# Kernel tuning notes

Measured on AMD Instinct MI355X. Metric: run time of the kernel, lower is better.

Reference implementation:

```python
import jax, jax.numpy as jnp
import numpy as np

MAX_DISP = 4  # 9x9 = 81 displacement window, stride 1


def setup_inputs() -> dict:
    key = jax.random.key(0)
    k1, k2 = jax.random.split(key)
    B, C, H, W = 4, 256, 128, 224
    first = jax.random.normal(k1, (B, C, H, W), dtype=jnp.float32)
    second = jax.random.normal(k2, (B, C, H, W), dtype=jnp.float32)
    return {"first": first, "second": second}


def reference(first, second):
    # FlowNet-style correlation: out[b, 9*dy+dx, y, x] =
    #   (1/C) * sum_c first[b,c,y,x] * second[b,c, y+dy-4, x+dx-4]
    # with zero padding outside the image (rbot buffers are zero-padded by 4).
    B, C, H, W = first.shape
    P = MAX_DISP
    sp = jnp.pad(second, ((0, 0), (0, 0), (P, P), (P, P)))  # [B,C,H+8,W+8]
    outs = []
    for dy in range(2 * P + 1):          # top channel = dy*9 + dx (dx fastest)
        for dx in range(2 * P + 1):
            shifted = sp[:, :, dy:dy + H, dx:dx + W]
            outs.append(jnp.sum(first * shifted, axis=1))  # [B,H,W]
    out = jnp.stack(outs, axis=1)  # [B,81,H,W]
    return out / jnp.float32(C)
```

## Files before the change

### kernel.cpp

```cpp
#include <hip/hip_runtime.h>

#define PAD   4
#define DD    9
#define ND    81
#define BB    4
#define CCH   256
#define HH_   128
#define WW_   224
#define TH    8
#define TW    32
#define NTILES 448
#define PLANE  (HH_*WW_)

__global__ __launch_bounds__(64)
void corr_kernel(const float* __restrict__ first,
                 const float* __restrict__ second,
                 const float* __restrict__ zws,
                 float* __restrict__ out)
{
    const int bx   = blockIdx.x;
    const int tile = bx % NTILES;
    const int dy   = bx / NTILES;
    const int wt   = tile % 7;
    const int ht   = (tile / 7) % 16;
    const int b    = tile / 112;
    const int w0   = wt * TW, h0 = ht * TH;

    const int lane = threadIdx.x;
    const int wq   = lane & 7;
    const int hh   = lane >> 3;

    const int h = h0 + hh;
    const int w = w0 + 4 * wq;
    const int srow  = h + dy - PAD;
    const bool valid = (srow >= 0) && (srow < HH_);
    const int srowc = valid ? srow : 0;

    const size_t plane = PLANE;
    const float* fbase = first  + (size_t)b * CCH * plane;
    const float* sbase = second + (size_t)b * CCH * plane;

    const float* fp = fbase + (size_t)h * WW_ + w;
    const float* sp = valid ? (sbase + (size_t)srowc * WW_ + w) : zws;
    const size_t sinc = valid ? plane : 0;

    const bool isL = (wq == 0), isR = (wq == 7);
    const int  ecol   = isL ? (w0 - PAD) : (w0 + TW);
    const bool evalid = valid && ((isL && w0 > 0) || (isR && (w0 + TW) < WW_));
    const float* ep = evalid ? (sbase + (size_t)srowc * WW_ + ecol) : zws;
    const size_t einc = evalid ? plane : 0;

    const int li = (lane + 63) & 63;
    const int ri = (lane + 1) & 63;

    float acc[DD][4];
    #pragma unroll
    for (int dx = 0; dx < DD; ++dx) { acc[dx][0]=0.f; acc[dx][1]=0.f; acc[dx][2]=0.f; acc[dx][3]=0.f; }

    float4 f = *(const float4*)fp;  fp += plane;
    float4 m = *(const float4*)sp;  sp += sinc;
    float4 e = *(const float4*)ep;  ep += einc;

    for (int c = 0; c < CCH; ++c) {
        float4 fn, mn, en;
        if (c + 1 < CCH) {
            fn = *(const float4*)fp;  fp += plane;
            mn = *(const float4*)sp;  sp += sinc;
            en = *(const float4*)ep;  ep += einc;
        } else { fn = f; mn = m; en = e; }

        float a0 = __shfl(m.x, li), a1 = __shfl(m.y, li),
              a2 = __shfl(m.z, li), a3 = __shfl(m.w, li);
        float c0 = __shfl(m.x, ri), c1 = __shfl(m.y, ri),
              c2 = __shfl(m.z, ri), c3 = __shfl(m.w, ri);
        if (isL) { a0 = e.x; a1 = e.y; a2 = e.z; a3 = e.w; }
        if (isR) { c0 = e.x; c1 = e.y; c2 = e.z; c3 = e.w; }

        const float s[12] = { a0, a1, a2, a3,
                              m.x, m.y, m.z, m.w,
                              c0, c1, c2, c3 };
        const float fv[4] = { f.x, f.y, f.z, f.w };

        #pragma unroll
        for (int dx = 0; dx < DD; ++dx)
            #pragma unroll
            for (int px = 0; px < 4; ++px)
                acc[dx][px] += fv[px] * s[dx + px];

        f = fn; m = mn; e = en;
    }

    const float inv = 1.0f / (float)CCH;
    #pragma unroll
    for (int dx = 0; dx < DD; ++dx) {
        const int d = dy * DD + dx;
        float4 o = make_float4(acc[dx][0]*inv, acc[dx][1]*inv,
                               acc[dx][2]*inv, acc[dx][3]*inv);
        *(float4*)&out[(((size_t)b * ND + d) * HH_ + h) * WW_ + w] = o;
    }
}

extern "C" void kernel_launch(void* const* d_in, const int* in_sizes, int n_in,
                              void* d_out, int out_size, void* d_ws, size_t ws_size,
                              hipStream_t stream) {
    const float* first  = (const float*)d_in[0];
    const float* second = (const float*)d_in[1];
    float* out = (float*)d_out;
    hipMemsetAsync(d_ws, 0, 256, stream);
    dim3 grid(NTILES * DD);
    dim3 block(64);
    corr_kernel<<<grid, block, 0, stream>>>(first, second, (const float*)d_ws, out);
}
```

Before: 459.9 us.

## Split the nine horizontal displacements across two wavefronts per block

Each block now runs two 64-lane wavefronts over the same pixel tile. Wave 0 computes displacements dx 0-3 and wave 1 computes dx 4-8, which cuts per-thread accumulators from 36 to 20 and raises the thread count. The cost is that both waves load the same first and second channels, roughly doubling global/L2 load traffic per output. Wave 0 also does a redundant fifth accumulator that it never stores.

```diff
diff --git a/kernel.cpp b/kernel.cpp
--- a/kernel.cpp
+++ b/kernel.cpp
@@ -12,7 +12,7 @@
 #define NTILES 448
 #define PLANE  (HH_*WW_)
 
-__global__ __launch_bounds__(64)
+__global__ __launch_bounds__(128)
 void corr_kernel(const float* __restrict__ first,
                  const float* __restrict__ second,
                  const float* __restrict__ zws,
@@ -26,7 +26,9 @@
     const int b    = tile / 112;
     const int w0   = wt * TW, h0 = ht * TH;
 
-    const int lane = threadIdx.x;
+    const int tid  = threadIdx.x;
+    const int wv   = tid >> 6;
+    const int lane = tid & 63;
     const int wq   = lane & 7;
     const int hh   = lane >> 3;
 
@@ -45,17 +47,23 @@
     const size_t sinc = valid ? plane : 0;
 
     const bool isL = (wq == 0), isR = (wq == 7);
-    const int  ecol   = isL ? (w0 - PAD) : (w0 + TW);
-    const bool evalid = valid && ((isL && w0 > 0) || (isR && (w0 + TW) < WW_));
+    const int  ecol   = wv ? (w0 + TW) : (w0 - PAD);
+    const bool evalid = valid && (wv ? (isR && (w0 + TW) < WW_)
+                                     : (isL && w0 > 0));
     const float* ep = evalid ? (sbase + (size_t)srowc * WW_ + ecol) : zws;
     const size_t einc = evalid ? plane : 0;
 
     const int li = (lane + 63) & 63;
     const int ri = (lane + 1) & 63;
 
-    float acc[DD][4];
+    const int sel_lo = wv ? lane : li;
+    const int sel_hi = wv ? ri   : lane;
+    const bool rep_lo = (wv == 0) && isL;
+    const bool rep_hi = (wv == 1) && isR;
+
+    float acc[5][4];
     #pragma unroll
-    for (int dx = 0; dx < DD; ++dx) { acc[dx][0]=0.f; acc[dx][1]=0.f; acc[dx][2]=0.f; acc[dx][3]=0.f; }
+    for (int j = 0; j < 5; ++j) { acc[j][0]=0.f; acc[j][1]=0.f; acc[j][2]=0.f; acc[j][3]=0.f; }
 
     float4 f = *(const float4*)fp;  fp += plane;
     float4 m = *(const float4*)sp;  sp += sinc;
@@ -69,33 +77,32 @@
             en = *(const float4*)ep;  ep += einc;
         } else { fn = f; mn = m; en = e; }
 
-        float a0 = __shfl(m.x, li), a1 = __shfl(m.y, li),
-              a2 = __shfl(m.z, li), a3 = __shfl(m.w, li);
-        float c0 = __shfl(m.x, ri), c1 = __shfl(m.y, ri),
-              c2 = __shfl(m.z, ri), c3 = __shfl(m.w, ri);
-        if (isL) { a0 = e.x; a1 = e.y; a2 = e.z; a3 = e.w; }
-        if (isR) { c0 = e.x; c1 = e.y; c2 = e.z; c3 = e.w; }
+        float t0 = __shfl(m.x, sel_lo), t1 = __shfl(m.y, sel_lo),
+              t2 = __shfl(m.z, sel_lo), t3 = __shfl(m.w, sel_lo);
+        float t4 = __shfl(m.x, sel_hi), t5 = __shfl(m.y, sel_hi),
+              t6 = __shfl(m.z, sel_hi), t7 = __shfl(m.w, sel_hi);
+        if (rep_lo) { t0 = e.x; t1 = e.y; t2 = e.z; t3 = e.w; }
+        if (rep_hi) { t4 = e.x; t5 = e.y; t6 = e.z; t7 = e.w; }
 
-        const float s[12] = { a0, a1, a2, a3,
-                              m.x, m.y, m.z, m.w,
-                              c0, c1, c2, c3 };
+        const float t[8]  = { t0, t1, t2, t3, t4, t5, t6, t7 };
         const float fv[4] = { f.x, f.y, f.z, f.w };
 
         #pragma unroll
-        for (int dx = 0; dx < DD; ++dx)
+        for (int j = 0; j < 5; ++j)
             #pragma unroll
             for (int px = 0; px < 4; ++px)
-                acc[dx][px] += fv[px] * s[dx + px];
+                acc[j][px] += fv[px] * t[j + px];
 
         f = fn; m = mn; e = en;
     }
 
     const float inv = 1.0f / (float)CCH;
     #pragma unroll
-    for (int dx = 0; dx < DD; ++dx) {
-        const int d = dy * DD + dx;
-        float4 o = make_float4(acc[dx][0]*inv, acc[dx][1]*inv,
-                               acc[dx][2]*inv, acc[dx][3]*inv);
+    for (int j = 0; j < 5; ++j) {
+        if (wv == 0 && j == 4) continue;
+        const int d = dy * DD + wv * 4 + j;
+        float4 o = make_float4(acc[j][0]*inv, acc[j][1]*inv,
+                               acc[j][2]*inv, acc[j][3]*inv);
         *(float4*)&out[(((size_t)b * ND + d) * HH_ + h) * WW_ + w] = o;
     }
 }
@@ -108,6 +115,6 @@
     float* out = (float*)d_out;
     hipMemsetAsync(d_ws, 0, 256, stream);
     dim3 grid(NTILES * DD);
-    dim3 block(64);
+    dim3 block(128);
     corr_kernel<<<grid, block, 0, stream>>>(first, second, (const float*)d_ws, out);
 }
```

After: 529.5 us. +15.1%, slower.
